# Performance work log

Measured on AMD Instinct MI355X. Metric: run time of the kernel, lower is better.

The kernel has to match this reference:

```python
import jax, jax.numpy as jnp
import numpy as np

D, H, COND, MLP_RATIO = 1024, 16, 1024, 4
HD = D // H
DFF = MLP_RATIO * D


def layer_norm(x, w, eps=1e-5):
    xf = x.astype(jnp.float32)
    mu = jnp.mean(xf, axis=-1, keepdims=True)
    var = jnp.mean((xf - mu) ** 2, axis=-1, keepdims=True)
    return (xf - mu) * jax.lax.rsqrt(var + eps) * w


def rms_norm(x, w, eps=1e-6):
    xf = x.astype(jnp.float32)
    rms = jnp.sqrt(jnp.mean(xf * xf, axis=-1, keepdims=True) + eps)
    return (xf / rms * w).astype(x.dtype)


def rotate_half(x):
    x1, x2 = x[..., : x.shape[-1] // 2], x[..., x.shape[-1] // 2:]
    return jnp.concatenate([-x2, x1], axis=-1)


def apply_rope(x, cos, sin):
    return x * cos + rotate_half(x) * sin


def setup_inputs() -> dict:
    key = jax.random.key(0)
    ks = jax.random.split(key, 16)
    B, S = 4, 2048
    pos = jnp.arange(S, dtype=jnp.float32)
    inv = 1.0 / (10000.0 ** (jnp.arange(0, HD, 2, dtype=jnp.float32) / HD))
    freqs = pos[:, None] * inv[None, :]              # (S, HD/2)
    emb = jnp.concatenate([freqs, freqs], axis=-1)   # (S, HD)
    return {
        "x": jax.random.normal(ks[0], (B, S, D), jnp.float32),
        "cos": jnp.cos(emb)[None, :, None, :],        # (1,S,1,HD)
        "sin": jnp.sin(emb)[None, :, None, :],
        "c": jax.random.normal(ks[1], (B, COND), jnp.float32),
        "norm1_w": jnp.ones((D,), jnp.float32),
        "Wqkv": jax.random.normal(ks[2], (D, 3 * D), jnp.float32) * 0.02,
        "Wout": jax.random.normal(ks[3], (D, D), jnp.float32) * 0.02,
        "q_norm_w": jnp.ones((HD,), jnp.float32),
        "k_norm_w": jnp.ones((HD,), jnp.float32),
        "norm2_w": jnp.ones((D,), jnp.float32),
        "W1": jax.random.normal(ks[4], (D, DFF), jnp.float32) * 0.02,
        "b1": jnp.zeros((DFF,), jnp.float32),
        "W2": jax.random.normal(ks[5], (DFF, D), jnp.float32) * 0.02,
        "b2": jnp.zeros((D,), jnp.float32),
        "ada_W": jax.random.normal(ks[6], (COND, 6 * D), jnp.float32) * 0.02,
        "ada_b": jnp.zeros((6 * D,), jnp.float32),
    }


def reference(x, cos, sin, c, norm1_w, Wqkv, Wout, q_norm_w, k_norm_w,
              norm2_w, W1, b1, W2, b2, ada_W, ada_b):
    B, S, _ = x.shape
    mod = (c @ ada_W + ada_b)[:, None, :]            # (B,1,6D)
    sh_msa, sc_msa, g_msa, sh_mlp, sc_mlp, g_mlp = jnp.split(mod, 6, axis=-1)

    x_norm = layer_norm(x, norm1_w) * (1 + sc_msa) + sh_msa
    qkv = (x_norm @ Wqkv).reshape(B, S, 3, H, HD)
    q, k, v = qkv[:, :, 0], qkv[:, :, 1], qkv[:, :, 2]  # (B,S,H,HD)
    q = apply_rope(rms_norm(q, q_norm_w), cos, sin)
    k = apply_rope(rms_norm(k, k_norm_w), cos, sin)

    scale = 1.0 / jnp.sqrt(jnp.float32(HD))
    logits = jnp.einsum('bqhd,bkhd->bhqk', q, k) * scale
    probs = jax.nn.softmax(logits, axis=-1)
    attn = jnp.einsum('bhqk,bkhd->bqhd', probs, v).reshape(B, S, D)

    x = x + g_msa * (attn @ Wout)

    x_norm = layer_norm(x, norm2_w) * (1 + sc_mlp) + sh_mlp
    h = jax.nn.gelu(x_norm @ W1 + b1, approximate=True)
    x = x + g_mlp * (h @ W2 + b2)
    return x
```

## Files before the change

kernel.cpp:

```cpp
#include <hip/hip_runtime.h>
#include <hip/hip_bf16.h>
#include <math.h>

typedef __bf16 bf16;
typedef __bf16 bf16x8 __attribute__((ext_vector_type(8)));
typedef __bf16 bf16x4 __attribute__((ext_vector_type(4)));
typedef float f32x4 __attribute__((ext_vector_type(4)));
typedef short s16x4 __attribute__((ext_vector_type(4)));

#define S_LEN 2048
#define NTOK 8192
#define DIM 1024
#define NH 16
#define HEADD 64
#define DFF 4096
#define MODD 6144

__device__ __forceinline__ float gelu_tanh(float x) {
  float inner = 0.7978845608028654f * (x + 0.044715f * x * x * x);
  return 0.5f * x * (1.0f + tanhf(inner));
}

__device__ __forceinline__ void gl_lds16(const bf16* g, bf16* l) {
  __builtin_amdgcn_global_load_lds(
      (const __attribute__((address_space(1))) unsigned int*)g,
      (__attribute__((address_space(3))) unsigned int*)l, 16, 0, 0);
}

__global__ __launch_bounds__(256) void init_mod_kernel(
    const float* __restrict__ ada_b, float* __restrict__ mod) {
  int i = blockIdx.x * 256 + threadIdx.x;
  mod[i] = ada_b[i % MODD];
}

__global__ __launch_bounds__(256) void ada_gemm_kernel(
    const float* __restrict__ cnd, const float* __restrict__ W,
    float* __restrict__ mod) {
  int n = blockIdx.x * 256 + threadIdx.x;
  int k0 = blockIdx.y * 128;
  float a0 = 0.f, a1 = 0.f, a2 = 0.f, a3 = 0.f;
  for (int k = k0; k < k0 + 128; ++k) {
    float w = W[(size_t)k * MODD + n];
    a0 = fmaf(cnd[k], w, a0);
    a1 = fmaf(cnd[1024 + k], w, a1);
    a2 = fmaf(cnd[2048 + k], w, a2);
    a3 = fmaf(cnd[3072 + k], w, a3);
  }
  atomicAdd(&mod[n], a0);
  atomicAdd(&mod[MODD + n], a1);
  atomicAdd(&mod[2 * MODD + n], a2);
  atomicAdd(&mod[3 * MODD + n], a3);
}

__global__ __launch_bounds__(256) void transpose_cast_kernel(
    const float* __restrict__ W, bf16* __restrict__ Wt, int K, int N) {
  __shared__ float tile[32][33];
  int n0 = blockIdx.x * 32, k0 = blockIdx.y * 32;
  int r = threadIdx.x >> 3;
  int c4 = (threadIdx.x & 7) * 4;
  float4 v = *(const float4*)&W[(size_t)(k0 + r) * N + n0 + c4];
  tile[r][c4 + 0] = v.x; tile[r][c4 + 1] = v.y;
  tile[r][c4 + 2] = v.z; tile[r][c4 + 3] = v.w;
  __syncthreads();
  bf16x4 o;
  o[0] = (bf16)tile[c4 + 0][r];
  o[1] = (bf16)tile[c4 + 1][r];
  o[2] = (bf16)tile[c4 + 2][r];
  o[3] = (bf16)tile[c4 + 3][r];
  *(bf16x4*)&Wt[(size_t)(n0 + r) * K + k0 + c4] = o;
}

__global__ __launch_bounds__(256) void vtrans_kernel(
    const bf16* __restrict__ qkv, bf16* __restrict__ VT) {
  __shared__ __align__(16) bf16 t[64][72];
  const int bh = blockIdx.y;
  const int b = bh >> 4, h = bh & 15;
  const int s0 = blockIdx.x * 64;
  const int tid = threadIdx.x;
  {
    const int r = tid >> 2;
    const int c = (tid & 3) * 16;
    const bf16* src =
        qkv + (size_t)(b * S_LEN + s0 + r) * 3072 + 2048 + h * 64 + c;
    *(bf16x8*)&t[r][c] = *(const bf16x8*)src;
    *(bf16x8*)&t[r][c + 8] = *(const bf16x8*)(src + 8);
  }
  __syncthreads();
  {
    const int d = tid & 63;
    const int sc = (tid >> 6) * 16;
    bf16x8 o0, o1;
#pragma unroll
    for (int j = 0; j < 8; ++j) o0[j] = t[sc + j][d];
#pragma unroll
    for (int j = 0; j < 8; ++j) o1[j] = t[sc + 8 + j][d];
    bf16* dst = VT + (size_t)(bh * 64 + d) * S_LEN + s0 + sc;
    *(bf16x8*)dst = o0;
    *(bf16x8*)(dst + 8) = o1;
  }
}

__global__ __launch_bounds__(256) void ln_mod_kernel(
    const float* __restrict__ x, const float* __restrict__ w,
    const float* __restrict__ mod, int sh_off, int sc_off,
    bf16* __restrict__ out) {
  __shared__ float red[8];
  const int row = blockIdx.x;
  const int b = row >> 11;
  const int tid = threadIdx.x;
  const float4 v = ((const float4*)(x + (size_t)row * DIM))[tid];
  float s1 = v.x + v.y + v.z + v.w;
  float s2 = v.x * v.x + v.y * v.y + v.z * v.z + v.w * v.w;
  for (int off = 32; off > 0; off >>= 1) {
    s1 += __shfl_down(s1, off, 64);
    s2 += __shfl_down(s2, off, 64);
  }
  const int wid = tid >> 6;
  if ((tid & 63) == 0) { red[wid] = s1; red[4 + wid] = s2; }
  __syncthreads();
  s1 = red[0] + red[1] + red[2] + red[3];
  s2 = red[4] + red[5] + red[6] + red[7];
  const float mu = s1 * (1.0f / DIM);
  const float inv = rsqrtf(s2 * (1.0f / DIM) - mu * mu + 1e-5f);
  const int c = tid * 4;
  const float* mb = mod + (size_t)b * MODD;
  float xs[4] = {v.x, v.y, v.z, v.w};
  bf16x4 o;
#pragma unroll
  for (int j = 0; j < 4; ++j)
    o[j] = (bf16)(((xs[j] - mu) * inv) * w[c + j] * (1.0f + mb[sc_off + c + j]) +
                  mb[sh_off + c + j]);
  *(bf16x4*)(out + (size_t)row * DIM + c) = o;
}

template <int EPI, int MT, int BN>
__global__ __launch_bounds__(256) void gemm_bt(
    const bf16* __restrict__ A, const bf16* __restrict__ Bt,
    bf16* __restrict__ Cb, float* __restrict__ Cf,
    const float* __restrict__ bias, const float* __restrict__ gmod,
    const float* __restrict__ resid, const float* __restrict__ cosb,
    const float* __restrict__ sinb, const float* __restrict__ qw,
    const float* __restrict__ kw, int M, int N, int K) {
  constexpr int IM = MT / 32;
  constexpr int JN = BN / 32;
  constexpr int AG = MT / 64;
  constexpr int BG = BN / 64;
  __shared__ __align__(16) bf16 As[MT * 32];
  __shared__ __align__(16) bf16 Bs[BN * 32];
  const int tid = threadIdx.x;
  const int wid = tid >> 6;
  const int lane = tid & 63;
  const int l15 = lane & 15;
  const int quad = lane >> 4;
  const int m0 = blockIdx.y * MT;
  const int n0 = blockIdx.x * BN;
  const int wm = (wid & 1) * (MT / 2);
  const int wn = (wid >> 1) * (BN / 2);

  const int srow = wid * 16 + (lane >> 2);
  const int scol = (lane & 3) * 8;
  const bf16* Ap = A + (size_t)(m0 + srow) * K + scol;
  const bf16* Bp = Bt + (size_t)(n0 + srow) * K + scol;

  f32x4 acc[IM][JN] = {};

  for (int kt = 0; kt < K; kt += 32) {
    __syncthreads();
#pragma unroll
    for (int g = 0; g < AG; ++g)
      gl_lds16(Ap + (size_t)g * 64 * K + kt, As + g * 2048 + wid * 512);
#pragma unroll
    for (int g = 0; g < BG; ++g)
      gl_lds16(Bp + (size_t)g * 64 * K + kt, Bs + g * 2048 + wid * 512);
    __syncthreads();

    bf16x8 af[IM], bfr[JN];
#pragma unroll
    for (int i = 0; i < IM; ++i)
      af[i] = *(const bf16x8*)&As[(wm + i * 16 + l15) * 32 + quad * 8];
#pragma unroll
    for (int j = 0; j < JN; ++j)
      bfr[j] = *(const bf16x8*)&Bs[(wn + j * 16 + l15) * 32 + quad * 8];
#pragma unroll
    for (int i = 0; i < IM; ++i)
#pragma unroll
      for (int j = 0; j < JN; ++j)
        acc[i][j] = __builtin_amdgcn_mfma_f32_16x16x32_bf16(af[i], bfr[j],
                                                            acc[i][j], 0, 0, 0);
  }

  if (EPI == 4 && n0 < 2048) {
    const float* nw = ((n0 + wn) < 1024) ? qw : kw;
    float wv[4];
#pragma unroll
    for (int j = 0; j < 4; ++j) wv[j] = nw[j * 16 + l15];
#pragma unroll
    for (int i = 0; i < IM; ++i) {
#pragma unroll
      for (int r = 0; r < 4; ++r) {
        const int m = m0 + wm + i * 16 + quad * 4 + r;
        const int s = m & (S_LEN - 1);
        float v[4];
        float ss = 0.f;
#pragma unroll
        for (int j = 0; j < 4; ++j) { v[j] = acc[i][j][r]; ss += v[j] * v[j]; }
        ss += __shfl_xor(ss, 1, 64);
        ss += __shfl_xor(ss, 2, 64);
        ss += __shfl_xor(ss, 4, 64);
        ss += __shfl_xor(ss, 8, 64);
        const float inv = rsqrtf(ss * (1.0f / HEADD) + 1e-6f);
        float xn[4];
#pragma unroll
        for (int j = 0; j < 4; ++j) xn[j] = v[j] * inv * wv[j];
#pragma unroll
        for (int j = 0; j < 4; ++j) {
          const int d = j * 16 + l15;
          const float rot = (j < 2) ? -xn[j + 2] : xn[j - 2];
          const float o = xn[j] * cosb[s * HEADD + d] + rot * sinb[s * HEADD + d];
          Cb[(size_t)m * N + n0 + wn + d] = (bf16)o;
        }
      }
    }
    return;
  }

#pragma unroll
  for (int i = 0; i < IM; ++i) {
#pragma unroll
    for (int r = 0; r < 4; ++r) {
      const int m = m0 + wm + i * 16 + quad * 4 + r;
#pragma unroll
      for (int j = 0; j < JN; ++j) {
        const int n = n0 + wn + j * 16 + l15;
        float v = acc[i][j][r];
        if (EPI == 0 || EPI == 4) {
          Cb[(size_t)m * N + n] = (bf16)v;
        } else if (EPI == 1) {
          const int b = m >> 11;
          Cf[(size_t)m * N + n] =
              resid[(size_t)m * N + n] + gmod[(size_t)b * MODD + n] * v;
        } else if (EPI == 2) {
          v += bias[n];
          Cb[(size_t)m * N + n] = (bf16)gelu_tanh(v);
        } else {
          v += bias[n];
          const int b = m >> 11;
          Cf[(size_t)m * N + n] =
              resid[(size_t)m * N + n] + gmod[(size_t)b * MODD + n] * v;
        }
      }
    }
  }
}

__global__ __launch_bounds__(256) void attn_kernel(
    const bf16* __restrict__ qkv, const bf16* __restrict__ VT,
    bf16* __restrict__ Opart, float* __restrict__ psumbuf) {
  __shared__ __align__(16) bf16 Ks[4096];
  __shared__ __align__(16) bf16 Vs[4096];
  const int bh = blockIdx.y;
  const int b = bh >> 4;
  const int h = bh & 15;
  const int q0 = blockIdx.x * 128;
  const int split = blockIdx.z;
  const int tid = threadIdx.x;
  const int wid = tid >> 6;
  const int lane = tid & 63;
  const int l15 = lane & 15;
  const int quad = lane >> 4;

  bf16x8 aq[2][2];
#pragma unroll
  for (int i = 0; i < 2; ++i) {
    const int qrow = q0 + wid * 32 + i * 16 + l15;
    const size_t qbase = (size_t)(b * S_LEN + qrow) * (3 * DIM) + h * HEADD;
    aq[i][0] = *(const bf16x8*)(qkv + qbase + quad * 8);
    aq[i][1] = *(const bf16x8*)(qkv + qbase + 32 + quad * 8);
  }

  const int rstage = lane;
  const int rsw = rstage & 7;
  const bf16* krow =
      qkv + (size_t)(b * S_LEN + split * 1024 + rstage) * 3072 + DIM + h * HEADD;
  const bf16* vrow = VT + (size_t)(bh * 64 + rstage) * S_LEN + split * 1024;

  bf16x8 kreg[2], vreg[2];
#pragma unroll
  for (int rr = 0; rr < 2; ++rr) {
    const int ck = wid + 4 * rr;
    kreg[rr] = *(const bf16x8*)(krow + ck * 8);
    vreg[rr] = *(const bf16x8*)(vrow + ck * 8);
  }

  const float cexp = 0.125f * 1.44269504f;
  f32x4 oacc[2][4] = {};
  float psum[2] = {0.f, 0.f};

  for (int t = 0; t < 16; ++t) {
    __syncthreads();
#pragma unroll
    for (int rr = 0; rr < 2; ++rr) {
      const int ck = wid + 4 * rr;
      const int sw = ((ck ^ rsw) << 3);
      *(bf16x8*)&Ks[rstage * 64 + sw] = kreg[rr];
      *(bf16x8*)&Vs[rstage * 64 + sw] = vreg[rr];
    }
    __syncthreads();
    if (t < 15) {
      krow += 64 * 3072;
      vrow += 64;
#pragma unroll
      for (int rr = 0; rr < 2; ++rr) {
        const int ck = wid + 4 * rr;
        kreg[rr] = *(const bf16x8*)(krow + ck * 8);
        vreg[rr] = *(const bf16x8*)(vrow + ck * 8);
      }
    }

    f32x4 sc[2][4] = {};
#pragma unroll
    for (int hh = 0; hh < 2; ++hh) {
#pragma unroll
      for (int cc = 0; cc < 4; ++cc) {
        const int row = cc * 16 + l15;
        const bf16x8 kf =
            *(const bf16x8*)&Ks[row * 64 + (((quad + 4 * hh) ^ (l15 & 7)) << 3)];
#pragma unroll
        for (int i = 0; i < 2; ++i)
          sc[i][cc] = __builtin_amdgcn_mfma_f32_16x16x32_bf16(kf, aq[i][hh],
                                                              sc[i][cc], 0, 0, 0);
      }
    }

    s16x4 pf[2][4];
#pragma unroll
    for (int i = 0; i < 2; ++i)
#pragma unroll
      for (int cc = 0; cc < 4; ++cc) {
        bf16x4 pb;
#pragma unroll
        for (int r = 0; r < 4; ++r) {
          const float p = __builtin_amdgcn_exp2f(fmaf(sc[i][cc][r], cexp, -8.0f));
          psum[i] += p;
          pb[r] = (bf16)p;
        }
        pf[i][cc] = __builtin_bit_cast(s16x4, pb);
      }

#pragma unroll
    for (int j = 0; j < 4; ++j) {
      const int d = 16 * j + l15;
      const int drow = d * 64;
      const int dsw = d & 7;
#pragma unroll
      for (int cc = 0; cc < 4; ++cc) {
        const int ck = 2 * cc + (quad >> 1);
        const s16x4 vf =
            *(const s16x4*)&Vs[drow + ((ck ^ dsw) << 3) + ((quad & 1) << 2)];
#pragma unroll
        for (int i = 0; i < 2; ++i)
          oacc[i][j] = __builtin_amdgcn_mfma_f32_16x16x16bf16_1k(pf[i][cc], vf,
                                                                 oacc[i][j], 0, 0, 0);
      }
    }
  }

#pragma unroll
  for (int i = 0; i < 2; ++i) {
    float ps = psum[i];
    ps += __shfl_xor(ps, 16, 64);
    ps += __shfl_xor(ps, 32, 64);
    if (lane < 16) {
      const int qrow = q0 + wid * 32 + i * 16 + lane;
      psumbuf[(size_t)split * (NTOK * NH) + (size_t)(b * S_LEN + qrow) * NH + h] = ps;
    }
#pragma unroll
    for (int r = 0; r < 4; ++r) {
      const int m = q0 + wid * 32 + i * 16 + quad * 4 + r;
#pragma unroll
      for (int j = 0; j < 4; ++j)
        Opart[(size_t)split * (NTOK * DIM) +
              ((size_t)(b * S_LEN + m) * NH + h) * HEADD + j * 16 + l15] =
            (bf16)oacc[i][j][r];
    }
  }
}

__global__ __launch_bounds__(256) void attn_reduce_kernel(
    const bf16* __restrict__ Opart, const float* __restrict__ psumbuf,
    bf16* __restrict__ attn) {
  const int g = blockIdx.x * 256 + threadIdx.x;
  const int token = g >> 7;
  const int rem = g & 127;
  const int h = rem >> 3;
  const int d0 = (rem & 7) * 8;
  const size_t off = ((size_t)token * NH + h) * HEADD + d0;
  const bf16x8 o0 = *(const bf16x8*)(Opart + off);
  const bf16x8 o1 = *(const bf16x8*)(Opart + (size_t)NTOK * DIM + off);
  const float l = psumbuf[token * NH + h] + psumbuf[NTOK * NH + token * NH + h];
  const float invl = 1.0f / l;
  bf16x8 o;
#pragma unroll
  for (int j = 0; j < 8; ++j)
    o[j] = (bf16)(((float)o0[j] + (float)o1[j]) * invl);
  *(bf16x8*)(attn + off) = o;
}

extern "C" void kernel_launch(void* const* d_in, const int* in_sizes, int n_in,
                              void* d_out, int out_size, void* d_ws,
                              size_t ws_size, hipStream_t stream) {
  const float* x = (const float*)d_in[0];
  const float* cosb = (const float*)d_in[1];
  const float* sinb = (const float*)d_in[2];
  const float* cnd = (const float*)d_in[3];
  const float* norm1_w = (const float*)d_in[4];
  const float* Wqkv = (const float*)d_in[5];
  const float* Wout = (const float*)d_in[6];
  const float* q_norm_w = (const float*)d_in[7];
  const float* k_norm_w = (const float*)d_in[8];
  const float* norm2_w = (const float*)d_in[9];
  const float* W1 = (const float*)d_in[10];
  const float* b1 = (const float*)d_in[11];
  const float* W2 = (const float*)d_in[12];
  const float* b2 = (const float*)d_in[13];
  const float* ada_W = (const float*)d_in[14];
  const float* ada_b = (const float*)d_in[15];
  float* out = (float*)d_out;

  char* p = (char*)d_ws;
  float* mod = (float*)p;   p += (size_t)4 * MODD * 4;
  bf16* WqkvT = (bf16*)p;   p += (size_t)3072 * 1024 * 2;
  bf16* WoutT = (bf16*)p;   p += (size_t)1024 * 1024 * 2;
  bf16* W1T = (bf16*)p;     p += (size_t)4096 * 1024 * 2;
  bf16* W2T = (bf16*)p;     p += (size_t)1024 * 4096 * 2;
  bf16* XN = (bf16*)p;      p += (size_t)NTOK * DIM * 2;
  bf16* QKV = (bf16*)p;     p += (size_t)NTOK * 3 * DIM * 2;
  bf16* ATTN = (bf16*)p;    p += (size_t)NTOK * DIM * 2;
  bf16* Hbuf = (bf16*)p;    p += (size_t)NTOK * DFF * 2;
  bf16* VT = Hbuf;
  bf16* Opart = Hbuf + (size_t)NTOK * DIM;
  float* psumbuf = (float*)(Hbuf + (size_t)3 * NTOK * DIM);

  init_mod_kernel<<<96, 256, 0, stream>>>(ada_b, mod);
  ada_gemm_kernel<<<dim3(24, 8), 256, 0, stream>>>(cnd, ada_W, mod);
  transpose_cast_kernel<<<dim3(96, 32), 256, 0, stream>>>(Wqkv, WqkvT, 1024, 3072);
  transpose_cast_kernel<<<dim3(32, 32), 256, 0, stream>>>(Wout, WoutT, 1024, 1024);
  transpose_cast_kernel<<<dim3(128, 32), 256, 0, stream>>>(W1, W1T, 1024, 4096);
  transpose_cast_kernel<<<dim3(32, 128), 256, 0, stream>>>(W2, W2T, 4096, 1024);
  ln_mod_kernel<<<NTOK, 256, 0, stream>>>(x, norm1_w, mod, 0, 1024, XN);
  gemm_bt<4, 128, 128><<<dim3(24, 64), 256, 0, stream>>>(
      XN, WqkvT, QKV, nullptr, nullptr, nullptr, nullptr, cosb, sinb,
      q_norm_w, k_norm_w, NTOK, 3072, 1024);
  vtrans_kernel<<<dim3(32, 64), 256, 0, stream>>>(QKV, VT);
  attn_kernel<<<dim3(16, 64, 2), 256, 0, stream>>>(QKV, VT, Opart, psumbuf);
  attn_reduce_kernel<<<4096, 256, 0, stream>>>(Opart, psumbuf, ATTN);
  gemm_bt<1, 128, 128><<<dim3(8, 64), 256, 0, stream>>>(
      ATTN, WoutT, nullptr, out, nullptr, mod + 2 * 1024, x, nullptr, nullptr,
      nullptr, nullptr, NTOK, 1024, 1024);
  ln_mod_kernel<<<NTOK, 256, 0, stream>>>(out, norm2_w, mod, 3 * 1024, 4 * 1024, XN);
  gemm_bt<2, 128, 128><<<dim3(32, 64), 256, 0, stream>>>(
      XN, W1T, Hbuf, nullptr, b1, nullptr, nullptr, nullptr, nullptr,
      nullptr, nullptr, NTOK, DFF, 1024);
  gemm_bt<3, 128, 128><<<dim3(8, 64), 256, 0, stream>>>(
      Hbuf, W2T, nullptr, out, b2, mod + 5 * 1024, out, nullptr, nullptr,
      nullptr, nullptr, NTOK, 1024, DFF);
  (void)in_sizes; (void)n_in; (void)out_size; (void)ws_size;
}
```

Baseline: 670.7 us.

## Double-buffer GEMM LDS tiles and use exp2/rcp fast GELU

The GEMM main loop now uses two LDS buffers per operand. It issues the global-to-LDS loads for the next K tile before computing MFMAs on the current one, leaving one barrier per iteration instead of two, so load latency overlaps compute. The GELU epilogue replaces tanhf with the equivalent form x*sigmoid(2u), computed with a hardware exp2 and reciprocal, which lowers epilogue cost at the price of slightly less accuracy. Doubling shared memory may reduce occupancy.

Measured after the change: 618.2 us. -7.8%, faster.

```diff
diff --git a/kernel.cpp b/kernel.cpp
--- a/kernel.cpp
+++ b/kernel.cpp
@@ -16,9 +16,10 @@
 #define DFF 4096
 #define MODD 6144
 
-__device__ __forceinline__ float gelu_tanh(float x) {
-  float inner = 0.7978845608028654f * (x + 0.044715f * x * x * x);
-  return 0.5f * x * (1.0f + tanhf(inner));
+__device__ __forceinline__ float gelu_fast(float x) {
+  float u = 0.7978845608028654f * (x + 0.044715f * x * x * x);
+  float e = __builtin_amdgcn_exp2f(-2.8853900817779268f * u);
+  return x * __builtin_amdgcn_rcpf(1.0f + e);
 }
 
 __device__ __forceinline__ void gl_lds16(const bf16* g, bf16* l) {
@@ -145,8 +146,8 @@
   constexpr int JN = BN / 32;
   constexpr int AG = MT / 64;
   constexpr int BG = BN / 64;
-  __shared__ __align__(16) bf16 As[MT * 32];
-  __shared__ __align__(16) bf16 Bs[BN * 32];
+  __shared__ __align__(16) bf16 As[2][MT * 32];
+  __shared__ __align__(16) bf16 Bs[2][BN * 32];
   const int tid = threadIdx.x;
   const int wid = tid >> 6;
   const int lane = tid & 63;
@@ -162,31 +163,46 @@
   const bf16* Ap = A + (size_t)(m0 + srow) * K + scol;
   const bf16* Bp = Bt + (size_t)(n0 + srow) * K + scol;
 
+#pragma unroll
+  for (int g = 0; g < AG; ++g)
+    gl_lds16(Ap + (size_t)g * 64 * K, As[0] + g * 2048 + wid * 512);
+#pragma unroll
+  for (int g = 0; g < BG; ++g)
+    gl_lds16(Bp + (size_t)g * 64 * K, Bs[0] + g * 2048 + wid * 512);
+  __syncthreads();
+
   f32x4 acc[IM][JN] = {};
+  int cur = 0;
 
   for (int kt = 0; kt < K; kt += 32) {
-    __syncthreads();
-#pragma unroll
-    for (int g = 0; g < AG; ++g)
-      gl_lds16(Ap + (size_t)g * 64 * K + kt, As + g * 2048 + wid * 512);
-#pragma unroll
-    for (int g = 0; g < BG; ++g)
-      gl_lds16(Bp + (size_t)g * 64 * K + kt, Bs + g * 2048 + wid * 512);
-    __syncthreads();
+    if (kt + 32 < K) {
+      const int nxt = cur ^ 1;
+#pragma unroll
+      for (int g = 0; g < AG; ++g)
+        gl_lds16(Ap + (size_t)g * 64 * K + kt + 32,
+                 As[nxt] + g * 2048 + wid * 512);
+#pragma unroll
+      for (int g = 0; g < BG; ++g)
+        gl_lds16(Bp + (size_t)g * 64 * K + kt + 32,
+                 Bs[nxt] + g * 2048 + wid * 512);
+    }
 
     bf16x8 af[IM], bfr[JN];
 #pragma unroll
     for (int i = 0; i < IM; ++i)
-      af[i] = *(const bf16x8*)&As[(wm + i * 16 + l15) * 32 + quad * 8];
+      af[i] = *(const bf16x8*)&As[cur][(wm + i * 16 + l15) * 32 + quad * 8];
 #pragma unroll
     for (int j = 0; j < JN; ++j)
-      bfr[j] = *(const bf16x8*)&Bs[(wn + j * 16 + l15) * 32 + quad * 8];
+      bfr[j] = *(const bf16x8*)&Bs[cur][(wn + j * 16 + l15) * 32 + quad * 8];
 #pragma unroll
     for (int i = 0; i < IM; ++i)
 #pragma unroll
       for (int j = 0; j < JN; ++j)
         acc[i][j] = __builtin_amdgcn_mfma_f32_16x16x32_bf16(af[i], bfr[j],
                                                             acc[i][j], 0, 0, 0);
+
+    __syncthreads();
+    cur ^= 1;
   }
 
   if (EPI == 4 && n0 < 2048) {
@@ -241,7 +257,7 @@
               resid[(size_t)m * N + n] + gmod[(size_t)b * MODD + n] * v;
         } else if (EPI == 2) {
           v += bias[n];
-          Cb[(size_t)m * N + n] = (bf16)gelu_tanh(v);
+          Cb[(size_t)m * N + n] = (bf16)gelu_fast(v);
         } else {
           v += bias[n];
           const int b = m >> 11;
```
